# Performance work log

Measured on AMD Instinct MI355X. Metric: run time of the kernel, lower is better.

Reference implementation:

```python
import jax, jax.numpy as jnp
import numpy as np

KERNEL = 3
PAD = (KERNEL - 1) // 2  # 'same' padding applied manually, conv itself is VALID


def _conv2d(x, w, padding):
    # x: (N,H,W,Cin), w: (kh,kw,Cin,Cout)
    return jax.lax.conv_general_dilated(
        x, w, window_strides=(1, 1), padding=padding,
        dimension_numbers=('NHWC', 'HWIO', 'NHWC'))


def convlstm2d(x, kernel, rec_kernel, bias):
    """Keras ConvLSTM2D (valid input conv on pre-padded input, SAME recurrent conv).

    x: (B,T,H,W,Cin); kernel: (k,k,Cin,4F); rec_kernel: (k,k,F,4F); bias: (4F,)
    Returns full hidden sequence (B,T,H,W,F).
    """
    # tf.pad with paddings [[0,0],[0,0],[p,p],[p,p],[0,0]] (constant mode)
    xp = jnp.pad(x, ((0, 0), (0, 0), (PAD, PAD), (PAD, PAD), (0, 0)))
    B, T = x.shape[:2]
    # Fuse the input-to-hidden conv across all timesteps in one big conv
    xz = _conv2d(xp.reshape((B * T,) + xp.shape[2:]), kernel, 'VALID') + bias
    H, W, F4 = xz.shape[1:]
    F = F4 // 4
    xz = xz.reshape(B, T, H, W, F4).transpose(1, 0, 2, 3, 4)  # (T,B,H,W,4F)

    def step(carry, xt):
        h, c = carry
        z = xt + _conv2d(h, rec_kernel, 'SAME')
        zi, zf, zc, zo = jnp.split(z, 4, axis=-1)  # Keras gate order i,f,c,o
        i = jax.nn.sigmoid(zi)
        f = jax.nn.sigmoid(zf)
        c = f * c + i * jnp.tanh(zc)
        o = jax.nn.sigmoid(zo)
        h = o * jnp.tanh(c)
        return (h, c), h

    h0 = jnp.zeros((B, H, W, F), x.dtype)
    (_, _), hs = jax.lax.scan(step, (h0, h0), xz)
    return hs.transpose(1, 0, 2, 3, 4)  # (B,T,H,W,F)


def setup_inputs() -> dict:
    key = jax.random.key(0)
    ks = jax.random.split(key, 7)
    B, T, H, W, Cin, F = 4, 16, 64, 64, 32, 32
    std = float(np.sqrt(2.0 / (KERNEL * KERNEL * F)))  # he-style kernel init
    x = jax.random.normal(ks[0], (B, T, H, W, Cin), jnp.float32)
    k1 = jax.random.normal(ks[1], (KERNEL, KERNEL, Cin, 4 * F), jnp.float32) * std
    rk1 = jax.random.normal(ks[2], (KERNEL, KERNEL, F, 4 * F), jnp.float32) * std
    b1 = jnp.zeros((4 * F,), jnp.float32)
    k2 = jax.random.normal(ks[3], (KERNEL, KERNEL, F, 4 * F), jnp.float32) * std
    rk2 = jax.random.normal(ks[4], (KERNEL, KERNEL, F, 4 * F), jnp.float32) * std
    b2 = jnp.zeros((4 * F,), jnp.float32)
    return {"x": x, "k1": k1, "rk1": rk1, "b1": b1, "k2": k2, "rk2": rk2, "b2": b2}


def reference(x, k1, rk1, b1, k2, rk2, b2):
    # normalization=None -> identity; pad + ConvLSTM2D, twice
    h = convlstm2d(x, k1, rk1, b1)
    h = convlstm2d(h, k2, rk2, b2)
    return h
```

## Files before the change

### kernel.cpp

```cpp
#include <hip/hip_runtime.h>


typedef __bf16 bf16x8 __attribute__((ext_vector_type(8)));
typedef float f32x4 __attribute__((ext_vector_type(4)));

#define WPK_ELEMS 73728
#define PLANE 524288

__device__ __forceinline__ float fsigmoid(float z) {
    return 1.0f / (1.0f + __expf(-z));
}
__device__ __forceinline__ float ftanh(float z) {
    z = fminf(15.0f, fmaxf(-15.0f, z));
    float e = __expf(2.0f * z);
    return (e - 1.0f) / (e + 1.0f);
}

__global__ __launch_bounds__(256) void pack_weights(
    const float* __restrict__ wk1, const float* __restrict__ wr1,
    const float* __restrict__ wk2, const float* __restrict__ wr2,
    __bf16* __restrict__ wpk)
{
    int i = blockIdx.x * 256 + threadIdx.x;
    if (i >= 2 * WPK_ELEMS) return;
    int layer = i / WPK_ELEMS;
    int r = i - layer * WPK_ELEMS;
    int j2 = r & 7;
    int L  = (r >> 3) & 63;
    int nt = (r >> 9) & 7;
    int cix = r >> 12;
    int tap = cix >> 1, src = cix & 1;
    int s = ((L >> 4) << 3) + j2;
    int gate = nt & 3;
    int f = ((nt >> 2) << 4) + (L & 15);
    int n = (gate << 5) + f;
    const float* w = layer ? (src ? wr2 : wk2) : (src ? wr1 : wk1);
    wpk[i] = (__bf16)w[(tap * 32 + s) * 128 + n];
}

__device__ __forceinline__ bf16x8 cvt8(const float* p) {
    const float4 f0 = *(const float4*)p;
    const float4 f1 = *(const float4*)(p + 4);
    bf16x8 v;
    v[0] = (__bf16)f0.x; v[1] = (__bf16)f0.y;
    v[2] = (__bf16)f0.z; v[3] = (__bf16)f0.w;
    v[4] = (__bf16)f1.x; v[5] = (__bf16)f1.y;
    v[6] = (__bf16)f1.z; v[7] = (__bf16)f1.w;
    return v;
}

#define MFMA16(A0, A1, A2, A3, WP, ACC)                                                   \
    {                                                                                     \
        const bf16x8 w0 = WP[0], w1 = WP[64], w2 = WP[128], w3 = WP[192];                 \
        ACC[0][0] = __builtin_amdgcn_mfma_f32_16x16x32_bf16(A0, w0, ACC[0][0], 0, 0, 0);  \
        ACC[0][1] = __builtin_amdgcn_mfma_f32_16x16x32_bf16(A0, w1, ACC[0][1], 0, 0, 0);  \
        ACC[0][2] = __builtin_amdgcn_mfma_f32_16x16x32_bf16(A0, w2, ACC[0][2], 0, 0, 0);  \
        ACC[0][3] = __builtin_amdgcn_mfma_f32_16x16x32_bf16(A0, w3, ACC[0][3], 0, 0, 0);  \
        ACC[1][0] = __builtin_amdgcn_mfma_f32_16x16x32_bf16(A1, w0, ACC[1][0], 0, 0, 0);  \
        ACC[1][1] = __builtin_amdgcn_mfma_f32_16x16x32_bf16(A1, w1, ACC[1][1], 0, 0, 0);  \
        ACC[1][2] = __builtin_amdgcn_mfma_f32_16x16x32_bf16(A1, w2, ACC[1][2], 0, 0, 0);  \
        ACC[1][3] = __builtin_amdgcn_mfma_f32_16x16x32_bf16(A1, w3, ACC[1][3], 0, 0, 0);  \
        ACC[2][0] = __builtin_amdgcn_mfma_f32_16x16x32_bf16(A2, w0, ACC[2][0], 0, 0, 0);  \
        ACC[2][1] = __builtin_amdgcn_mfma_f32_16x16x32_bf16(A2, w1, ACC[2][1], 0, 0, 0);  \
        ACC[2][2] = __builtin_amdgcn_mfma_f32_16x16x32_bf16(A2, w2, ACC[2][2], 0, 0, 0);  \
        ACC[2][3] = __builtin_amdgcn_mfma_f32_16x16x32_bf16(A2, w3, ACC[2][3], 0, 0, 0);  \
        ACC[3][0] = __builtin_amdgcn_mfma_f32_16x16x32_bf16(A3, w0, ACC[3][0], 0, 0, 0);  \
        ACC[3][1] = __builtin_amdgcn_mfma_f32_16x16x32_bf16(A3, w1, ACC[3][1], 0, 0, 0);  \
        ACC[3][2] = __builtin_amdgcn_mfma_f32_16x16x32_bf16(A3, w2, ACC[3][2], 0, 0, 0);  \
        ACC[3][3] = __builtin_amdgcn_mfma_f32_16x16x32_bf16(A3, w3, ACC[3][3], 0, 0, 0);  \
    }

__global__ __launch_bounds__(1024, 1) void clstm_m64(
    const float* __restrict__ x,
    const __bf16* __restrict__ wpk1, const __bf16* __restrict__ wpk2,
    const float* __restrict__ bias1, const float* __restrict__ bias2,
    __bf16* __restrict__ h1buf,
    __bf16* __restrict__ h2buf,
    float* __restrict__ c1,
    float* __restrict__ c2,
    float* __restrict__ out, int j)
{
    __shared__ __bf16 tXA[6 * 66 * 36];
    __shared__ __bf16 tRA[6 * 66 * 36];
    __shared__ __bf16 tXB[4 * 66 * 36];
    __shared__ __bf16 tHA[4 * 66 * 36];
    __shared__ float  cpass[2 * 64 * 32];

    const int blk = blockIdx.x;
    const int k = blk >> 3;
    const int layer = k >> 4;
    if (layer ? (j < 1) : (j > 7)) return;
    const int grp = (blk & 7) * 16 + (k & 15);
    const int T0 = layer ? (2 * j - 2) : (2 * j);
    const int R = grp << 1;
    const int b = R >> 6, y0 = R & 63;

    const int tid = threadIdx.x;
    const int wid = tid >> 6, L = tid & 63;
    const int c = L & 15, q = L >> 4, q8 = q * 8;

    const bf16x8* wpkv = (const bf16x8*)(layer ? wpk2 : wpk1);
    const float* bias = layer ? bias2 : bias1;
    float* cl = layer ? c2 : c1;

    const float*  xA  = x + (size_t)(b * 16 + T0) * 131072;
    const float*  xB  = xA + 131072;
    const __bf16* h1A = h1buf + (size_t)(T0 & 3) * PLANE;
    const __bf16* h1B = h1buf + (size_t)((T0 + 1) & 3) * PLANE;
    const __bf16* hRA = layer ? (h2buf + (size_t)(((T0 - 1) >> 1) & 1) * PLANE)
                              : (h1buf + (size_t)((T0 - 1) & 3) * PLANE);

    const int n1 = T0 ? 3168 : 1584;
    for (int i = tid; i < n1; i += 1024) {
        const int tile = (i >= 1584);
        const int r2 = i - tile * 1584;
        const int g = r2 & 3;
        const int rc = r2 >> 2;
        const int cc = rc % 66;
        const int row = rc / 66;
        const int yy = y0 - 2 + row;
        const int xc = cc - 1;
        bf16x8 v = {};
        if ((unsigned)yy < 64u && (unsigned)xc < 64u) {
            if (!layer && !tile) {
                v = cvt8(xA + ((size_t)yy * 64 + xc) * 32 + g * 8);
            } else {
                const __bf16* s = tile ? hRA : h1A;
                v = *(const bf16x8*)(s + (((size_t)(b * 64 + yy)) * 64 + xc) * 32 + g * 8);
            }
        }
        *(bf16x8*)((tile ? tRA : tXA) + (row * 66 + cc) * 36 + g * 8) = v;
    }
    for (int i = tid; i < 1056; i += 1024) {
        const int g = i & 3;
        const int rc = i >> 2;
        const int cc = rc % 66;
        const int row = rc / 66;
        const int yy = y0 - 1 + row;
        const int xc = cc - 1;
        bf16x8 v = {};
        if ((unsigned)yy < 64u && (unsigned)xc < 64u) {
            if (!layer) v = cvt8(xB + ((size_t)yy * 64 + xc) * 32 + g * 8);
            else        v = *(const bf16x8*)(h1B + (((size_t)(b * 64 + yy)) * 64 + xc) * 32 + g * 8);
        }
        *(bf16x8*)(tXB + (row * 66 + cc) * 36 + g * 8) = v;
    }
    for (int i = tid; i < 1188; i += 1024)
        *(bf16x8*)(tHA + i * 8) = (bf16x8){};
    __syncthreads();

    f32x4 accB[4][4];

    if (wid < 8) {
        const int wr = wid >> 1, fh = wid & 1;
        const int f = fh * 16 + c;
        const int ra = y0 - 1 + wr;
        const bool rv = ((unsigned)ra < 64u);
        if (rv) {
            float bv[4];
            #pragma unroll
            for (int g = 0; g < 4; ++g) bv[g] = bias[g * 32 + f];

            f32x4 acc[4][4];
            #pragma unroll
            for (int m = 0; m < 4; ++m)
                #pragma unroll
                for (int g = 0; g < 4; ++g)
                    acc[m][g] = (f32x4){bv[g], bv[g], bv[g], bv[g]};

            #pragma unroll
            for (int tap = 0; tap < 9; ++tap) {
                const int dyk = tap / 3, dxk = tap - dyk * 3;
                const int lb = ((wr + dyk) * 66 + c + dxk) * 36 + q8;
                {
                    const bf16x8 a0 = *(const bf16x8*)(tXA + lb);
                    const bf16x8 a1 = *(const bf16x8*)(tXA + lb + 16 * 36);
                    const bf16x8 a2 = *(const bf16x8*)(tXA + lb + 32 * 36);
                    const bf16x8 a3 = *(const bf16x8*)(tXA + lb + 48 * 36);
                    const bf16x8* wp = wpkv + (size_t)((tap * 2) * 8 + fh * 4) * 64 + L;
                    MFMA16(a0, a1, a2, a3, wp, acc);
                }
                if (T0 > 0) {
                    const bf16x8 h0 = *(const bf16x8*)(tRA + lb);
                    const bf16x8 h1v = *(const bf16x8*)(tRA + lb + 16 * 36);
                    const bf16x8 h2v = *(const bf16x8*)(tRA + lb + 32 * 36);
                    const bf16x8 h3v = *(const bf16x8*)(tRA + lb + 48 * 36);
                    const bf16x8* wp = wpkv + (size_t)((tap * 2 + 1) * 8 + fh * 4) * 64 + L;
                    MFMA16(h0, h1v, h2v, h3v, wp, acc);
                }
            }

            const bool own = (wr == 1 || wr == 2);
            const float* crd = cl + (size_t)((j - 1) & 1) * PLANE;
            const size_t rowA = (size_t)(b * 64 + ra) * 2048;
            #pragma unroll
            for (int m = 0; m < 4; ++m) {
                #pragma unroll
                for (int r = 0; r < 4; ++r) {
                    const int px = m * 16 + q * 4 + r;
                    const float ig = fsigmoid(acc[m][0][r]);
                    const float fg = fsigmoid(acc[m][1][r]);
                    const float gg = ftanh(acc[m][2][r]);
                    const float og = fsigmoid(acc[m][3][r]);
                    const float cold = T0 ? crd[rowA + (size_t)px * 32 + f] : 0.0f;
                    const float cn = (T0 ? fg * cold : 0.0f) + ig * gg;
                    const float hv = og * ftanh(cn);
                    tHA[(wr * 66 + px + 1) * 36 + f] = (__bf16)hv;
                    if (own) {
                        cpass[(wr - 1) * 2048 + px * 32 + f] = cn;
                        if (layer)
                            out[((size_t)(b * 16 + T0) * 4096 + (size_t)ra * 64 + px) * 32 + f] = hv;
                        else
                            h1buf[(size_t)(T0 & 3) * PLANE + rowA + (size_t)px * 32 + f] = (__bf16)hv;
                    }
                }
            }
        }
    } else if (wid < 12) {
        const int u = wid - 8;
        const int o = u >> 1, fh = u & 1;
        const int f = fh * 16 + c;
        float bv[4];
        #pragma unroll
        for (int g = 0; g < 4; ++g) bv[g] = bias[g * 32 + f];
        #pragma unroll
        for (int m = 0; m < 4; ++m)
            #pragma unroll
            for (int g = 0; g < 4; ++g)
                accB[m][g] = (f32x4){bv[g], bv[g], bv[g], bv[g]};

        #pragma unroll
        for (int tap = 0; tap < 9; ++tap) {
            const int dyk = tap / 3, dxk = tap - dyk * 3;
            const int lb = ((o + dyk) * 66 + c + dxk) * 36 + q8;
            const bf16x8 a0 = *(const bf16x8*)(tXB + lb);
            const bf16x8 a1 = *(const bf16x8*)(tXB + lb + 16 * 36);
            const bf16x8 a2 = *(const bf16x8*)(tXB + lb + 32 * 36);
            const bf16x8 a3 = *(const bf16x8*)(tXB + lb + 48 * 36);
            const bf16x8* wp = wpkv + (size_t)((tap * 2) * 8 + fh * 4) * 64 + L;
            MFMA16(a0, a1, a2, a3, wp, accB);
        }
    }
    __syncthreads();

    if (wid >= 8 && wid < 12) {
        const int u = wid - 8;
        const int o = u >> 1, fh = u & 1;
        const int f = fh * 16 + c;
        #pragma unroll
        for (int tap = 0; tap < 9; ++tap) {
            const int dyk = tap / 3, dxk = tap - dyk * 3;
            const int lb = ((o + dyk) * 66 + c + dxk) * 36 + q8;
            const bf16x8 h0 = *(const bf16x8*)(tHA + lb);
            const bf16x8 h1v = *(const bf16x8*)(tHA + lb + 16 * 36);
            const bf16x8 h2v = *(const bf16x8*)(tHA + lb + 32 * 36);
            const bf16x8 h3v = *(const bf16x8*)(tHA + lb + 48 * 36);
            const bf16x8* wp = wpkv + (size_t)((tap * 2 + 1) * 8 + fh * 4) * 64 + L;
            MFMA16(h0, h1v, h2v, h3v, wp, accB);
        }
        const int rb = y0 + o;
        float* cwr = cl + (size_t)(j & 1) * PLANE;
        __bf16* h2w = h2buf + (size_t)(((T0 + 1) >> 1) & 1) * PLANE;
        const size_t rowB = (size_t)(b * 64 + rb) * 2048;
        #pragma unroll
        for (int m = 0; m < 4; ++m) {
            #pragma unroll
            for (int r = 0; r < 4; ++r) {
                const int px = m * 16 + q * 4 + r;
                const float ig = fsigmoid(accB[m][0][r]);
                const float fg = fsigmoid(accB[m][1][r]);
                const float gg = ftanh(accB[m][2][r]);
                const float og = fsigmoid(accB[m][3][r]);
                const float cold = cpass[o * 2048 + px * 32 + f];
                const float cn = fg * cold + ig * gg;
                const float hv = og * ftanh(cn);
                cwr[rowB + (size_t)px * 32 + f] = cn;
                if (layer) {
                    out[((size_t)(b * 16 + T0 + 1) * 4096 + (size_t)rb * 64 + px) * 32 + f] = hv;
                    h2w[rowB + (size_t)px * 32 + f] = (__bf16)hv;
                } else {
                    h1buf[(size_t)((T0 + 1) & 3) * PLANE + rowB + (size_t)px * 32 + f] = (__bf16)hv;
                }
            }
        }
    }
}

extern "C" void kernel_launch(void* const* d_in, const int* in_sizes, int n_in,
                              void* d_out, int out_size, void* d_ws, size_t ws_size,
                              hipStream_t stream)
{
    const float* x   = (const float*)d_in[0];
    const float* k1  = (const float*)d_in[1];
    const float* rk1 = (const float*)d_in[2];
    const float* b1  = (const float*)d_in[3];
    const float* k2  = (const float*)d_in[4];
    const float* rk2 = (const float*)d_in[5];
    const float* b2  = (const float*)d_in[6];
    float* out = (float*)d_out;

    __bf16* wpk1  = (__bf16*)d_ws;
    __bf16* wpk2  = wpk1 + WPK_ELEMS;
    __bf16* h1buf = wpk2 + WPK_ELEMS;
    __bf16* h2buf = h1buf + 4 * (size_t)PLANE;
    float*  c1    = (float*)(h2buf + 2 * (size_t)PLANE);
    float*  c2    = c1 + 2 * (size_t)PLANE;

    pack_weights<<<(2 * WPK_ELEMS + 255) / 256, 256, 0, stream>>>(k1, rk1, k2, rk2, wpk1);

    for (int j = 0; j <= 8; ++j) {
        clstm_m64<<<256, 1024, 0, stream>>>(
            x, wpk1, wpk2, b1, b2, h1buf, h2buf, c1, c2, out, j);
    }
}
```

Before: 245.3 us.

## Overlap recurrent-tile staging with input-conv MFMAs via warp specialization

The first phase now stages only the input tiles (tXA, tXB) before a barrier. Waves 0-11 then run all input-to-hidden convolution MFMAs, while waves 12-15 load the recurrent-state tile tRA from global memory and zero tHA. After a second barrier, the recurrent MFMAs for the first timestep are applied on top of the same accumulators. The goal is to hide the global latency of loading recurrent state behind tensor-core work, at the cost of an extra barrier and fewer threads doing that load.

```diff
diff --git a/kernel.cpp b/kernel.cpp
--- a/kernel.cpp
+++ b/kernel.cpp
@@ -70,7 +70,7 @@
         ACC[3][3] = __builtin_amdgcn_mfma_f32_16x16x32_bf16(A3, w3, ACC[3][3], 0, 0, 0);  \
     }
 
-__global__ __launch_bounds__(1024, 1) void clstm_m64(
+__global__ __launch_bounds__(1024, 1) void clstm_v17(
     const float* __restrict__ x,
     const __bf16* __restrict__ wpk1, const __bf16* __restrict__ wpk2,
     const float* __restrict__ bias1, const float* __restrict__ bias2,
@@ -98,6 +98,10 @@
     const int tid = threadIdx.x;
     const int wid = tid >> 6, L = tid & 63;
     const int c = L & 15, q = L >> 4, q8 = q * 8;
+    const int fh = wid & 1;
+    const int f = fh * 16 + c;
+    const int wr = wid >> 1;
+    const int o  = wr - 4;
 
     const bf16x8* wpkv = (const bf16x8*)(layer ? wpk2 : wpk1);
     const float* bias = layer ? bias2 : bias1;
@@ -110,86 +114,113 @@
     const __bf16* hRA = layer ? (h2buf + (size_t)(((T0 - 1) >> 1) & 1) * PLANE)
                               : (h1buf + (size_t)((T0 - 1) & 3) * PLANE);
 
-    const int n1 = T0 ? 3168 : 1584;
-    for (int i = tid; i < n1; i += 1024) {
-        const int tile = (i >= 1584);
-        const int r2 = i - tile * 1584;
+    for (int i = tid; i < 2640; i += 1024) {
+        const int tb = (i >= 1584);
+        const int r2 = tb ? (i - 1584) : i;
         const int g = r2 & 3;
         const int rc = r2 >> 2;
         const int cc = rc % 66;
         const int row = rc / 66;
-        const int yy = y0 - 2 + row;
+        const int yy = (tb ? y0 - 1 : y0 - 2) + row;
         const int xc = cc - 1;
         bf16x8 v = {};
         if ((unsigned)yy < 64u && (unsigned)xc < 64u) {
-            if (!layer && !tile) {
-                v = cvt8(xA + ((size_t)yy * 64 + xc) * 32 + g * 8);
+            if (!layer) {
+                v = cvt8((tb ? xB : xA) + ((size_t)yy * 64 + xc) * 32 + g * 8);
             } else {
-                const __bf16* s = tile ? hRA : h1A;
+                const __bf16* s = tb ? h1B : h1A;
                 v = *(const bf16x8*)(s + (((size_t)(b * 64 + yy)) * 64 + xc) * 32 + g * 8);
             }
         }
-        *(bf16x8*)((tile ? tRA : tXA) + (row * 66 + cc) * 36 + g * 8) = v;
-    }
-    for (int i = tid; i < 1056; i += 1024) {
-        const int g = i & 3;
-        const int rc = i >> 2;
-        const int cc = rc % 66;
-        const int row = rc / 66;
-        const int yy = y0 - 1 + row;
-        const int xc = cc - 1;
-        bf16x8 v = {};
-        if ((unsigned)yy < 64u && (unsigned)xc < 64u) {
-            if (!layer) v = cvt8(xB + ((size_t)yy * 64 + xc) * 32 + g * 8);
-            else        v = *(const bf16x8*)(h1B + (((size_t)(b * 64 + yy)) * 64 + xc) * 32 + g * 8);
-        }
-        *(bf16x8*)(tXB + (row * 66 + cc) * 36 + g * 8) = v;
-    }
-    for (int i = tid; i < 1188; i += 1024)
-        *(bf16x8*)(tHA + i * 8) = (bf16x8){};
+        *(bf16x8*)((tb ? tXB : tXA) + (row * 66 + cc) * 36 + g * 8) = v;
+    }
     __syncthreads();
 
-    f32x4 accB[4][4];
+    f32x4 accU[4][4];
 
     if (wid < 8) {
-        const int wr = wid >> 1, fh = wid & 1;
-        const int f = fh * 16 + c;
+        const int ra = y0 - 1 + wr;
+        if ((unsigned)ra < 64u) {
+            float bv[4];
+            #pragma unroll
+            for (int g = 0; g < 4; ++g) bv[g] = bias[g * 32 + f];
+            #pragma unroll
+            for (int m = 0; m < 4; ++m)
+                #pragma unroll
+                for (int g = 0; g < 4; ++g)
+                    accU[m][g] = (f32x4){bv[g], bv[g], bv[g], bv[g]};
+
+            #pragma unroll
+            for (int tap = 0; tap < 9; ++tap) {
+                const int dyk = tap / 3, dxk = tap - dyk * 3;
+                const int lb = ((wr + dyk) * 66 + c + dxk) * 36 + q8;
+                const bf16x8 a0 = *(const bf16x8*)(tXA + lb);
+                const bf16x8 a1 = *(const bf16x8*)(tXA + lb + 16 * 36);
+                const bf16x8 a2 = *(const bf16x8*)(tXA + lb + 32 * 36);
+                const bf16x8 a3 = *(const bf16x8*)(tXA + lb + 48 * 36);
+                const bf16x8* wp = wpkv + (size_t)((tap * 2) * 8 + fh * 4) * 64 + L;
+                MFMA16(a0, a1, a2, a3, wp, accU);
+            }
+        }
+    } else if (wid < 12) {
+        float bv[4];
+        #pragma unroll
+        for (int g = 0; g < 4; ++g) bv[g] = bias[g * 32 + f];
+        #pragma unroll
+        for (int m = 0; m < 4; ++m)
+            #pragma unroll
+            for (int g = 0; g < 4; ++g)
+                accU[m][g] = (f32x4){bv[g], bv[g], bv[g], bv[g]};
+
+        #pragma unroll
+        for (int tap = 0; tap < 9; ++tap) {
+            const int dyk = tap / 3, dxk = tap - dyk * 3;
+            const int lb = ((o + dyk) * 66 + c + dxk) * 36 + q8;
+            const bf16x8 a0 = *(const bf16x8*)(tXB + lb);
+            const bf16x8 a1 = *(const bf16x8*)(tXB + lb + 16 * 36);
+            const bf16x8 a2 = *(const bf16x8*)(tXB + lb + 32 * 36);
+            const bf16x8 a3 = *(const bf16x8*)(tXB + lb + 48 * 36);
+            const bf16x8* wp = wpkv + (size_t)((tap * 2) * 8 + fh * 4) * 64 + L;
+            MFMA16(a0, a1, a2, a3, wp, accU);
+        }
+    } else {
+        const int t2 = tid - 768;
+        if (T0 > 0) {
+            for (int i = t2; i < 1584; i += 256) {
+                const int g = i & 3;
+                const int rc = i >> 2;
+                const int cc = rc % 66;
+                const int row = rc / 66;
+                const int yy = y0 - 2 + row;
+                const int xc = cc - 1;
+                bf16x8 v = {};
+                if ((unsigned)yy < 64u && (unsigned)xc < 64u)
+                    v = *(const bf16x8*)(hRA + (((size_t)(b * 64 + yy)) * 64 + xc) * 32 + g * 8);
+                *(bf16x8*)(tRA + (row * 66 + cc) * 36 + g * 8) = v;
+            }
+        }
+        for (int i = t2; i < 1188; i += 256)
+            *(bf16x8*)(tHA + i * 8) = (bf16x8){};
+    }
+    __syncthreads();
+
+    if (wid < 8) {
         const int ra = y0 - 1 + wr;
         const bool rv = ((unsigned)ra < 64u);
         if (rv) {
-            float bv[4];
-            #pragma unroll
-            for (int g = 0; g < 4; ++g) bv[g] = bias[g * 32 + f];
-
-            f32x4 acc[4][4];
-            #pragma unroll
-            for (int m = 0; m < 4; ++m)
+            if (T0 > 0) {
                 #pragma unroll
-                for (int g = 0; g < 4; ++g)
-                    acc[m][g] = (f32x4){bv[g], bv[g], bv[g], bv[g]};
-
-            #pragma unroll
-            for (int tap = 0; tap < 9; ++tap) {
-                const int dyk = tap / 3, dxk = tap - dyk * 3;
-                const int lb = ((wr + dyk) * 66 + c + dxk) * 36 + q8;
-                {
-                    const bf16x8 a0 = *(const bf16x8*)(tXA + lb);
-                    const bf16x8 a1 = *(const bf16x8*)(tXA + lb + 16 * 36);
-                    const bf16x8 a2 = *(const bf16x8*)(tXA + lb + 32 * 36);
-                    const bf16x8 a3 = *(const bf16x8*)(tXA + lb + 48 * 36);
-                    const bf16x8* wp = wpkv + (size_t)((tap * 2) * 8 + fh * 4) * 64 + L;
-                    MFMA16(a0, a1, a2, a3, wp, acc);
-                }
-                if (T0 > 0) {
+                for (int tap = 0; tap < 9; ++tap) {
+                    const int dyk = tap / 3, dxk = tap - dyk * 3;
+                    const int lb = ((wr + dyk) * 66 + c + dxk) * 36 + q8;
                     const bf16x8 h0 = *(const bf16x8*)(tRA + lb);
                     const bf16x8 h1v = *(const bf16x8*)(tRA + lb + 16 * 36);
                     const bf16x8 h2v = *(const bf16x8*)(tRA + lb + 32 * 36);
                     const bf16x8 h3v = *(const bf16x8*)(tRA + lb + 48 * 36);
                     const bf16x8* wp = wpkv + (size_t)((tap * 2 + 1) * 8 + fh * 4) * 64 + L;
-                    MFMA16(h0, h1v, h2v, h3v, wp, acc);
+                    MFMA16(h0, h1v, h2v, h3v, wp, accU);
                 }
             }
-
             const bool own = (wr == 1 || wr == 2);
             const float* crd = cl + (size_t)((j - 1) & 1) * PLANE;
             const size_t rowA = (size_t)(b * 64 + ra) * 2048;
@@ -198,10 +229,10 @@
                 #pragma unroll
                 for (int r = 0; r < 4; ++r) {
                     const int px = m * 16 + q * 4 + r;
-                    const float ig = fsigmoid(acc[m][0][r]);
-                    const float fg = fsigmoid(acc[m][1][r]);
-                    const float gg = ftanh(acc[m][2][r]);
-                    const float og = fsigmoid(acc[m][3][r]);
+                    const float ig = fsigmoid(accU[m][0][r]);
+                    const float fg = fsigmoid(accU[m][1][r]);
+                    const float gg = ftanh(accU[m][2][r]);
+                    const float og = fsigmoid(accU[m][3][r]);
                     const float cold = T0 ? crd[rowA + (size_t)px * 32 + f] : 0.0f;
                     const float cn = (T0 ? fg * cold : 0.0f) + ig * gg;
                     const float hv = og * ftanh(cn);
@@ -216,37 +247,10 @@
                 }
             }
         }
-    } else if (wid < 12) {
-        const int u = wid - 8;
-        const int o = u >> 1, fh = u & 1;
-        const int f = fh * 16 + c;
-        float bv[4];
-        #pragma unroll
-        for (int g = 0; g < 4; ++g) bv[g] = bias[g * 32 + f];
-        #pragma unroll
-        for (int m = 0; m < 4; ++m)
-            #pragma unroll
-            for (int g = 0; g < 4; ++g)
-                accB[m][g] = (f32x4){bv[g], bv[g], bv[g], bv[g]};
-
-        #pragma unroll
-        for (int tap = 0; tap < 9; ++tap) {
-            const int dyk = tap / 3, dxk = tap - dyk * 3;
-            const int lb = ((o + dyk) * 66 + c + dxk) * 36 + q8;
-            const bf16x8 a0 = *(const bf16x8*)(tXB + lb);
-            const bf16x8 a1 = *(const bf16x8*)(tXB + lb + 16 * 36);
-            const bf16x8 a2 = *(const bf16x8*)(tXB + lb + 32 * 36);
-            const bf16x8 a3 = *(const bf16x8*)(tXB + lb + 48 * 36);
-            const bf16x8* wp = wpkv + (size_t)((tap * 2) * 8 + fh * 4) * 64 + L;
-            MFMA16(a0, a1, a2, a3, wp, accB);
-        }
     }
     __syncthreads();
 
     if (wid >= 8 && wid < 12) {
-        const int u = wid - 8;
-        const int o = u >> 1, fh = u & 1;
-        const int f = fh * 16 + c;
         #pragma unroll
         for (int tap = 0; tap < 9; ++tap) {
             const int dyk = tap / 3, dxk = tap - dyk * 3;
@@ -256,7 +260,7 @@
             const bf16x8 h2v = *(const bf16x8*)(tHA + lb + 32 * 36);
             const bf16x8 h3v = *(const bf16x8*)(tHA + lb + 48 * 36);
             const bf16x8* wp = wpkv + (size_t)((tap * 2 + 1) * 8 + fh * 4) * 64 + L;
-            MFMA16(h0, h1v, h2v, h3v, wp, accB);
+            MFMA16(h0, h1v, h2v, h3v, wp, accU);
         }
         const int rb = y0 + o;
         float* cwr = cl + (size_t)(j & 1) * PLANE;
@@ -267,10 +271,10 @@
             #pragma unroll
             for (int r = 0; r < 4; ++r) {
                 const int px = m * 16 + q * 4 + r;
-                const float ig = fsigmoid(accB[m][0][r]);
-                const float fg = fsigmoid(accB[m][1][r]);
-                const float gg = ftanh(accB[m][2][r]);
-                const float og = fsigmoid(accB[m][3][r]);
+                const float ig = fsigmoid(accU[m][0][r]);
+                const float fg = fsigmoid(accU[m][1][r]);
+                const float gg = ftanh(accU[m][2][r]);
+                const float og = fsigmoid(accU[m][3][r]);
                 const float cold = cpass[o * 2048 + px * 32 + f];
                 const float cn = fg * cold + ig * gg;
                 const float hv = og * ftanh(cn);
@@ -309,7 +313,7 @@
     pack_weights<<<(2 * WPK_ELEMS + 255) / 256, 256, 0, stream>>>(k1, rk1, k2, rk2, wpk1);
 
     for (int j = 0; j <= 8; ++j) {
-        clstm_m64<<<256, 1024, 0, stream>>>(
+        clstm_v17<<<256, 1024, 0, stream>>>(
             x, wpk1, wpk2, b1, b2, h1buf, h2buf, c1, c2, out, j);
     }
 }
```

New measurement: 230.2 us (median of 2 runs). 1.07x faster.
